# Kernel tuning notes

Hardware: AMD Instinct MI355X
Metric: run time of the kernel (lower is better)

The kernel has to match this reference:

```python
import jax, jax.numpy as jnp
import numpy as np

N = 1_000_000
D_IN = 128
D_OUT = 128
S = 65_536


def setup_inputs() -> dict:
    key = jax.random.key(0)
    k1, k2, k3, k4 = jax.random.split(key, 4)
    element_embeddings = jax.random.normal(k1, (N, D_IN), dtype=jnp.float32)
    element_to_sample_map = jnp.sort(
        jax.random.randint(k2, (N,), 0, S, dtype=jnp.int64)
    )
    # nn.Linear(D_IN, 1, bias=False) weight -> vector [D_IN]
    w_att = jax.random.normal(k3, (D_IN,), dtype=jnp.float32) * (1.0 / np.sqrt(D_IN))
    # nn.Linear(D_IN, D_OUT, bias=False) weight [D_OUT, D_IN]
    w_out = jax.random.normal(k4, (D_OUT, D_IN), dtype=jnp.float32) * (1.0 / np.sqrt(D_IN))
    return {
        "element_embeddings": element_embeddings,
        "element_to_sample_map": element_to_sample_map,
        "num_samples": S,
        "w_att": w_att,
        "w_out": w_out,
    }


def reference(element_embeddings, element_to_sample_map, num_samples, w_att, w_out):
    seg = element_to_sample_map
    # attention scores [N]
    scores = element_embeddings @ w_att
    # segment log-softmax (numerically stable, single max/sum pass)
    seg_max = jax.ops.segment_max(scores, seg, num_segments=num_samples)
    shifted = scores - seg_max[seg]
    exp_shifted = jnp.exp(shifted)
    seg_sum = jax.ops.segment_sum(exp_shifted, seg, num_segments=num_samples)
    log_probs = shifted - jnp.log(seg_sum)[seg]
    attention_probs = jnp.exp(log_probs)  # [N]
    # output projection then weighted scatter-sum per segment -> [S, D_OUT]
    projected = element_embeddings @ w_out.T
    return jax.ops.segment_sum(
        projected * attention_probs[:, None], seg, num_segments=num_samples
    )
```

## Files before the change

### kernel.cpp

```cpp
#include <hip/hip_runtime.h>
#include <hip/hip_bf16.h>

#define N_ELEM 1000000
#define D 128
#define S_SEG 65536
#define SEGW 8
#define NBLK 2048
#define NEG_BIG (-1e30f)

#define DPP_ADD(v, CTRL) \
    v += __int_as_float(__builtin_amdgcn_update_dpp(0, __float_as_int(v), CTRL, 0xF, 0xF, true))

__device__ __forceinline__ void pairScores(float partial, float& s0, float& s1) {
    float v = partial;
    DPP_ADD(v, 0x111);
    DPP_ADD(v, 0x112);
    DPP_ADD(v, 0x114);
    DPP_ADD(v, 0x118);
    DPP_ADD(v, 0x142);
    s0 = __int_as_float(__builtin_amdgcn_readlane(__float_as_int(v), 31));
    s1 = __int_as_float(__builtin_amdgcn_readlane(__float_as_int(v), 63));
}

__device__ __forceinline__ float dot4(float4 v, float4 w) {
    return fmaf(v.x, w.x, fmaf(v.y, w.y, fmaf(v.z, w.z, v.w * w.w)));
}

__device__ __forceinline__ void osm_step(float& m, float& l, float4& a,
                                         float d, float4 v, bool valid) {
    float mn = valid ? fmaxf(m, d) : m;
    float scale = __expf(m - mn);
    float p = valid ? __expf(d - mn) : 0.f;
    m = mn;
    l = fmaf(l, scale, p);
    a.x = fmaf(a.x, scale, p * v.x);
    a.y = fmaf(a.y, scale, p * v.y);
    a.z = fmaf(a.z, scale, p * v.z);
    a.w = fmaf(a.w, scale, p * v.w);
}

__device__ __forceinline__ void osm_merge(float& m1, float& l1, float4& a1,
                                          float m2, float l2, float4 a2) {
    float m = fmaxf(m1, m2);
    float s1 = __expf(m1 - m), s2 = __expf(m2 - m);
    l1 = l1 * s1 + l2 * s2;
    a1.x = a1.x * s1 + a2.x * s2;
    a1.y = a1.y * s1 + a2.y * s2;
    a1.z = a1.z * s1 + a2.z * s2;
    a1.w = a1.w * s1 + a2.w * s2;
    m1 = m;
}

__global__ __launch_bounds__(256, 6) void k_fused(
        const float* __restrict__ emb, const int* __restrict__ seg,
        const float* __restrict__ watt, float* __restrict__ out) {
    const int lane = threadIdx.x & 63;
    const int half = lane >> 5;
    const int hl   = lane & 31;
    const int wid  = blockIdx.x * 4 + (threadIdx.x >> 6);
    const float4 wv = reinterpret_cast<const float4*>(watt)[hl];
    const float4* emb4 = reinterpret_cast<const float4*>(emb);
    float4* out4 = reinterpret_cast<float4*>(out);

    const int s0 = wid * SEGW;
    int lo = 0;
    if (lane <= SEGW) {
        const int target = s0 + lane;
        int hi = N_ELEM;
        while (lo < hi) {
            int mid = (lo + hi) >> 1;
            if (seg[mid] < target) lo = mid + 1; else hi = mid;
        }
    }

    #pragma unroll 1
    for (int si = 0; si < SEGW; ++si) {
        const int beg = __shfl(lo, si, 64);
        const int end = __shfl(lo, si + 1, 64);
        float  mA = NEG_BIG, lA = 0.f; float4 aA = {0.f, 0.f, 0.f, 0.f};
        float  mB = NEG_BIG, lB = 0.f; float4 aB = {0.f, 0.f, 0.f, 0.f};
        if (beg < end) {
            float4 c0 = emb4[(size_t)min(beg +     half, N_ELEM - 1) * 32 + hl];
            float4 c1 = emb4[(size_t)min(beg + 2 + half, N_ELEM - 1) * 32 + hl];
            float4 c2 = emb4[(size_t)min(beg + 4 + half, N_ELEM - 1) * 32 + hl];
            float4 c3 = emb4[(size_t)min(beg + 6 + half, N_ELEM - 1) * 32 + hl];
            #pragma unroll 1
            for (int e = beg; e < end; e += 4) {
                float4 n0 = emb4[(size_t)min(e + 8  + half, N_ELEM - 1) * 32 + hl];
                float4 n1 = emb4[(size_t)min(e + 10 + half, N_ELEM - 1) * 32 + hl];
                float s0a, s1a, s0b, s1b;
                pairScores(dot4(c0, wv), s0a, s1a);
                pairScores(dot4(c1, wv), s0b, s1b);
                float d0 = half ? s1a : s0a;
                float d1 = half ? s1b : s0b;
                osm_step(mA, lA, aA, d0, c0, (e +     half) < end);
                osm_step(mB, lB, aB, d1, c1, (e + 2 + half) < end);
                c0 = c2; c1 = c3; c2 = n0; c3 = n1;
            }
        }
        osm_merge(mA, lA, aA, mB, lB, aB);
        float  mo  = __shfl_xor(mA, 32, 64);
        float  lo2 = __shfl_xor(lA, 32, 64);
        float4 ao;
        ao.x = __shfl_xor(aA.x, 32, 64);
        ao.y = __shfl_xor(aA.y, 32, 64);
        ao.z = __shfl_xor(aA.z, 32, 64);
        ao.w = __shfl_xor(aA.w, 32, 64);
        osm_merge(mA, lA, aA, mo, lo2, ao);
        float inv = (lA > 0.f) ? 1.0f / lA : 0.f;
        if (half == 0) {
            float4 r = {aA.x * inv, aA.y * inv, aA.z * inv, aA.w * inv};
            out4[(size_t)(s0 + si) * 32 + hl] = r;
        }
    }
}

#define KT 32
#define PADR 132
__global__ __launch_bounds__(256, 4) void k_proj(
        float* __restrict__ out, const float* __restrict__ wout) {
    __shared__ float As[KT][PADR];
    __shared__ float Bs[KT][PADR];
    const int tid = threadIdx.x;
    const int r0 = blockIdx.x * 128;
    const int tx = tid & 15, ty = tid >> 4;
    const int rr = ty * 8, cc = tx * 8;
    float acc[8][8] = {};

    for (int kt = 0; kt < D / KT; ++kt) {
        #pragma unroll
        for (int i = 0; i < 4; ++i) {
            int idx = tid + i * 256;
            int r = idx >> 3, k4 = idx & 7;
            float4 a = *reinterpret_cast<const float4*>(
                &out[(size_t)(r0 + r) * D + kt * KT + k4 * 4]);
            float4 b = *reinterpret_cast<const float4*>(
                &wout[(size_t)r * D + kt * KT + k4 * 4]);
            As[k4 * 4 + 0][r] = a.x; As[k4 * 4 + 1][r] = a.y;
            As[k4 * 4 + 2][r] = a.z; As[k4 * 4 + 3][r] = a.w;
            Bs[k4 * 4 + 0][r] = b.x; Bs[k4 * 4 + 1][r] = b.y;
            Bs[k4 * 4 + 2][r] = b.z; Bs[k4 * 4 + 3][r] = b.w;
        }
        __syncthreads();
        #pragma unroll
        for (int kk = 0; kk < KT; ++kk) {
            float a[8], b[8];
            *reinterpret_cast<float4*>(&a[0]) = *reinterpret_cast<const float4*>(&As[kk][rr]);
            *reinterpret_cast<float4*>(&a[4]) = *reinterpret_cast<const float4*>(&As[kk][rr + 4]);
            *reinterpret_cast<float4*>(&b[0]) = *reinterpret_cast<const float4*>(&Bs[kk][cc]);
            *reinterpret_cast<float4*>(&b[4]) = *reinterpret_cast<const float4*>(&Bs[kk][cc + 4]);
            #pragma unroll
            for (int i = 0; i < 8; ++i)
                #pragma unroll
                for (int j = 0; j < 8; ++j)
                    acc[i][j] = fmaf(a[i], b[j], acc[i][j]);
        }
        __syncthreads();
    }
    #pragma unroll
    for (int i = 0; i < 8; ++i) {
        float4 o0 = {acc[i][0], acc[i][1], acc[i][2], acc[i][3]};
        float4 o1 = {acc[i][4], acc[i][5], acc[i][6], acc[i][7]};
        *reinterpret_cast<float4*>(&out[(size_t)(r0 + rr + i) * D + cc])     = o0;
        *reinterpret_cast<float4*>(&out[(size_t)(r0 + rr + i) * D + cc + 4]) = o1;
    }
}

extern "C" void kernel_launch(void* const* d_in, const int* in_sizes, int n_in,
                              void* d_out, int out_size, void* d_ws, size_t ws_size,
                              hipStream_t stream) {
    const float* emb  = (const float*)d_in[0];
    const int*   seg  = (const int*)d_in[1];
    const float* watt = (const float*)d_in[3];
    const float* wout = (const float*)d_in[4];
    float* out = (float*)d_out;

    k_fused<<<NBLK, 256, 0, stream>>>(emb, seg, watt, out);
    k_proj <<<S_SEG / 128, 256, 0, stream>>>(out, wout);
}
```

Baseline: 166.2 us.

## Stream elements across segment boundaries with one full-wave row per element

```diff
diff --git a/kernel.cpp b/kernel.cpp
--- a/kernel.cpp
+++ b/kernel.cpp
@@ -11,108 +11,98 @@
 #define DPP_ADD(v, CTRL) \
     v += __int_as_float(__builtin_amdgcn_update_dpp(0, __float_as_int(v), CTRL, 0xF, 0xF, true))
 
-__device__ __forceinline__ void pairScores(float partial, float& s0, float& s1) {
-    float v = partial;
+__device__ __forceinline__ float reduce64(float v) {
     DPP_ADD(v, 0x111);
     DPP_ADD(v, 0x112);
     DPP_ADD(v, 0x114);
     DPP_ADD(v, 0x118);
     DPP_ADD(v, 0x142);
-    s0 = __int_as_float(__builtin_amdgcn_readlane(__float_as_int(v), 31));
-    s1 = __int_as_float(__builtin_amdgcn_readlane(__float_as_int(v), 63));
+    DPP_ADD(v, 0x143);
+    return __int_as_float(__builtin_amdgcn_readlane(__float_as_int(v), 63));
 }
 
-__device__ __forceinline__ float dot4(float4 v, float4 w) {
-    return fmaf(v.x, w.x, fmaf(v.y, w.y, fmaf(v.z, w.z, v.w * w.w)));
-}
-
-__device__ __forceinline__ void osm_step(float& m, float& l, float4& a,
-                                         float d, float4 v, bool valid) {
-    float mn = valid ? fmaxf(m, d) : m;
-    float scale = __expf(m - mn);
-    float p = valid ? __expf(d - mn) : 0.f;
+__device__ __forceinline__ void osm2(float& m, float& l, float2& a,
+                                     float d, float2 v) {
+    float mn = fmaxf(m, d);
+    float sc = __expf(m - mn);
+    float p  = __expf(d - mn);
     m = mn;
-    l = fmaf(l, scale, p);
-    a.x = fmaf(a.x, scale, p * v.x);
-    a.y = fmaf(a.y, scale, p * v.y);
-    a.z = fmaf(a.z, scale, p * v.z);
-    a.w = fmaf(a.w, scale, p * v.w);
-}
-
-__device__ __forceinline__ void osm_merge(float& m1, float& l1, float4& a1,
-                                          float m2, float l2, float4 a2) {
-    float m = fmaxf(m1, m2);
-    float s1 = __expf(m1 - m), s2 = __expf(m2 - m);
-    l1 = l1 * s1 + l2 * s2;
-    a1.x = a1.x * s1 + a2.x * s2;
-    a1.y = a1.y * s1 + a2.y * s2;
-    a1.z = a1.z * s1 + a2.z * s2;
-    a1.w = a1.w * s1 + a2.w * s2;
-    m1 = m;
+    l = fmaf(l, sc, p);
+    a.x = fmaf(a.x, sc, p * v.x);
+    a.y = fmaf(a.y, sc, p * v.y);
 }
 
 __global__ __launch_bounds__(256, 6) void k_fused(
         const float* __restrict__ emb, const int* __restrict__ seg,
         const float* __restrict__ watt, float* __restrict__ out) {
     const int lane = threadIdx.x & 63;
-    const int half = lane >> 5;
-    const int hl   = lane & 31;
     const int wid  = blockIdx.x * 4 + (threadIdx.x >> 6);
-    const float4 wv = reinterpret_cast<const float4*>(watt)[hl];
-    const float4* emb4 = reinterpret_cast<const float4*>(emb);
-    float4* out4 = reinterpret_cast<float4*>(out);
+    const float2 wv = reinterpret_cast<const float2*>(watt)[lane];
+    const float2* emb2 = reinterpret_cast<const float2*>(emb);
+    float2* out2 = reinterpret_cast<float2*>(out);
 
     const int s0 = wid * SEGW;
     int lo = 0;
     if (lane <= SEGW) {
-        const int target = s0 + lane;
-        int hi = N_ELEM;
+        int target = s0 + lane, hi = N_ELEM;
         while (lo < hi) {
             int mid = (lo + hi) >> 1;
             if (seg[mid] < target) lo = mid + 1; else hi = mid;
         }
     }
 
+    int si = 0;
+    int e      = __shfl(lo, 0, 64);
+    int endCur = __shfl(lo, 1, 64);
+
+    float mA = NEG_BIG, lA = 0.f; float2 aA = {0.f, 0.f};
+    float mB = NEG_BIG, lB = 0.f; float2 aB = {0.f, 0.f};
+
+    float2 r0 = emb2[(size_t)min(e + 0, N_ELEM - 1) * 64 + lane];
+    float2 r1 = emb2[(size_t)min(e + 1, N_ELEM - 1) * 64 + lane];
+    float2 r2 = emb2[(size_t)min(e + 2, N_ELEM - 1) * 64 + lane];
+    float2 r3 = emb2[(size_t)min(e + 3, N_ELEM - 1) * 64 + lane];
+    int p = e + 4;
+
+#define FIN() do {                                                        \
+        float mm = fmaxf(mA, mB);                                         \
+        float w1 = __expf(mA - mm), w2 = __expf(mB - mm);                 \
+        float ll = lA * w1 + lB * w2;                                     \
+        float inv = (ll > 0.f) ? 1.0f / ll : 0.f;                         \
+        float2 r;                                                         \
+        r.x = (aA.x * w1 + aB.x * w2) * inv;                              \
+        r.y = (aA.y * w1 + aB.y * w2) * inv;                              \
+        out2[(size_t)(s0 + si) * 64 + lane] = r;                          \
+        mA = mB = NEG_BIG; lA = lB = 0.f;                                 \
+        aA.x = aA.y = aB.x = aB.y = 0.f;                                  \
+        ++si;                                                             \
+        if (si < SEGW) endCur = __shfl(lo, si + 1, 64);                   \
+    } while (0)
+
+#define SLOT(R, MS, LS, AS) do {                                          \
+        while (si < SEGW && e == endCur) FIN();                           \
+        if (si < SEGW) {                                                  \
+            float d = reduce64(fmaf(R.x, wv.x, R.y * wv.y));              \
+            osm2(MS, LS, AS, d, R);                                       \
+            ++e;                                                          \
+        }                                                                 \
+    } while (0)
+
     #pragma unroll 1
-    for (int si = 0; si < SEGW; ++si) {
-        const int beg = __shfl(lo, si, 64);
-        const int end = __shfl(lo, si + 1, 64);
-        float  mA = NEG_BIG, lA = 0.f; float4 aA = {0.f, 0.f, 0.f, 0.f};
-        float  mB = NEG_BIG, lB = 0.f; float4 aB = {0.f, 0.f, 0.f, 0.f};
-        if (beg < end) {
-            float4 c0 = emb4[(size_t)min(beg +     half, N_ELEM - 1) * 32 + hl];
-            float4 c1 = emb4[(size_t)min(beg + 2 + half, N_ELEM - 1) * 32 + hl];
-            float4 c2 = emb4[(size_t)min(beg + 4 + half, N_ELEM - 1) * 32 + hl];
-            float4 c3 = emb4[(size_t)min(beg + 6 + half, N_ELEM - 1) * 32 + hl];
-            #pragma unroll 1
-            for (int e = beg; e < end; e += 4) {
-                float4 n0 = emb4[(size_t)min(e + 8  + half, N_ELEM - 1) * 32 + hl];
-                float4 n1 = emb4[(size_t)min(e + 10 + half, N_ELEM - 1) * 32 + hl];
-                float s0a, s1a, s0b, s1b;
-                pairScores(dot4(c0, wv), s0a, s1a);
-                pairScores(dot4(c1, wv), s0b, s1b);
-                float d0 = half ? s1a : s0a;
-                float d1 = half ? s1b : s0b;
-                osm_step(mA, lA, aA, d0, c0, (e +     half) < end);
-                osm_step(mB, lB, aB, d1, c1, (e + 2 + half) < end);
-                c0 = c2; c1 = c3; c2 = n0; c3 = n1;
-            }
-        }
-        osm_merge(mA, lA, aA, mB, lB, aB);
-        float  mo  = __shfl_xor(mA, 32, 64);
-        float  lo2 = __shfl_xor(lA, 32, 64);
-        float4 ao;
-        ao.x = __shfl_xor(aA.x, 32, 64);
-        ao.y = __shfl_xor(aA.y, 32, 64);
-        ao.z = __shfl_xor(aA.z, 32, 64);
-        ao.w = __shfl_xor(aA.w, 32, 64);
-        osm_merge(mA, lA, aA, mo, lo2, ao);
-        float inv = (lA > 0.f) ? 1.0f / lA : 0.f;
-        if (half == 0) {
-            float4 r = {aA.x * inv, aA.y * inv, aA.z * inv, aA.w * inv};
-            out4[(size_t)(s0 + si) * 32 + hl] = r;
-        }
+    while (si < SEGW) {
+        float2 n0 = emb2[(size_t)min(p + 0, N_ELEM - 1) * 64 + lane];
+        float2 n1 = emb2[(size_t)min(p + 1, N_ELEM - 1) * 64 + lane];
+        float2 n2 = emb2[(size_t)min(p + 2, N_ELEM - 1) * 64 + lane];
+        float2 n3 = emb2[(size_t)min(p + 3, N_ELEM - 1) * 64 + lane];
+        p += 4;
+        SLOT(r0, mA, lA, aA);
+        SLOT(r1, mB, lB, aB);
+        SLOT(r2, mA, lA, aA);
+        SLOT(r3, mB, lB, aB);
+        r0 = n0; r1 = n1; r2 = n2; r3 = n3;
     }
+#undef SLOT
+#undef FIN
 }
 
 #define KT 32
```

Result: no change. 163.1 us (-1.9%).
